# Kernel tuning notes

Measured on AMD Instinct MI355X. Metric: run time of the kernel, lower is better.

## Reference

```python
import jax, jax.numpy as jnp
import numpy as np

REG_TOPK = 4
REG_CHANNELS = 64
ADD_MEAN = True
TOTAL_DIM = REG_TOPK + (1 if ADD_MEAN else 0)  # 5


def setup_inputs() -> dict:
    key = jax.random.key(0)
    k1, k2, k3 = jax.random.split(key, 3)
    N, C, H, W = 32, 32, 160, 160  # C = 4*(reg_max+1), reg_max=7
    x = jax.random.normal(k1, (N, C, H, W), dtype=jnp.float32)
    # 1x1 conv params, init std=0.01, bias 0 (as in torch module)
    w1 = jax.random.normal(k2, (REG_CHANNELS, 4 * TOTAL_DIM), dtype=jnp.float32) * 0.01
    b1 = jnp.zeros((REG_CHANNELS,), dtype=jnp.float32)
    w2 = jax.random.normal(k3, (1, REG_CHANNELS), dtype=jnp.float32) * 0.01
    b2 = jnp.zeros((1,), dtype=jnp.float32)
    return {"x": x, "w1": w1, "b1": b1, "w2": w2, "b2": b2}


def reference(x, w1, b1, w2, b2):
    N, C, H, W = x.shape
    bins = C // 4
    # softmax over distribution bins; move bins to last axis for top_k
    p = jax.nn.softmax(x.reshape(N, 4, bins, H, W), axis=2)  # (N,4,bins,H,W)
    p = jnp.transpose(p, (0, 1, 3, 4, 2))                    # (N,4,H,W,bins)
    topk, _ = jax.lax.top_k(p, REG_TOPK)                     # (N,4,H,W,k)
    if ADD_MEAN:
        stat = jnp.concatenate([topk, topk.mean(axis=-1, keepdims=True)], axis=-1)
    else:
        stat = topk                                          # (N,4,H,W,total_dim)
    # reshape to (N, 4*total_dim, H, W) matching torch layout (4, total_dim contiguous)
    stat = jnp.transpose(stat, (0, 1, 4, 2, 3)).reshape(N, 4 * TOTAL_DIM, H, W)
    y = jax.nn.relu(jnp.einsum('nchw,oc->nohw', stat, w1) + b1[None, :, None, None])
    y = jax.nn.sigmoid(jnp.einsum('nchw,oc->nohw', y, w2) + b2[None, :, None, None])
    return y
```

## Files before the change

kernel.cpp:

```cpp
#include <hip/hip_runtime.h>

#define HW_ 25600
#define CHW_ (32 * 25600)
#define NPIX 819200
#define ROWH 24

typedef _Float16 f16x8 __attribute__((ext_vector_type(8)));
typedef _Float16 h2 __attribute__((ext_vector_type(2)));
typedef float f32x4 __attribute__((ext_vector_type(4)));

__device__ __forceinline__ unsigned short h2us(_Float16 h) {
    return __builtin_bit_cast(unsigned short, h);
}
__device__ __forceinline__ unsigned packlo(h2 a, h2 b) {
    h2 r = {a.x, b.x};
    return __builtin_bit_cast(unsigned, r);
}
__device__ __forceinline__ unsigned packhi(h2 a, h2 b) {
    h2 r = {a.y, b.y};
    return __builtin_bit_cast(unsigned, r);
}
__device__ __forceinline__ h2 pkrtz(float a, float b) {
    return __builtin_bit_cast(h2, __builtin_amdgcn_cvt_pkrtz(a, b));
}

__global__ void dgqp_prep(const float* __restrict__ w1,
                          const float* __restrict__ b1,
                          unsigned short* __restrict__ w1f) {
    int t = threadIdx.x;
    int lane = t & 63;
    int col = ((t >> 6) << 4) | (lane & 15);
    int kg = lane >> 4;
    unsigned int pk[4];
    #pragma unroll
    for (int pr = 0; pr < 4; ++pr) {
        unsigned short hh[2];
        #pragma unroll
        for (int e = 0; e < 2; ++e) {
            int k = kg * 8 + pr * 2 + e;
            float v = 0.f;
            if (k < 16) {
                int g = k >> 2, idx = k & 3;
                v = w1[col * 20 + g * 5 + idx] + 0.25f * w1[col * 20 + g * 5 + 4];
            } else if (k == 16) {
                v = b1[col];
            }
            hh[e] = h2us((_Float16)v);
        }
        pk[pr] = (unsigned int)hh[0] | ((unsigned int)hh[1] << 16);
    }
    *reinterpret_cast<uint4*>(w1f + t * 8) = make_uint4(pk[0], pk[1], pk[2], pk[3]);
}

__global__ __launch_bounds__(256) void dgqp_main(
    const float* __restrict__ x,
    const unsigned short* __restrict__ w1f,
    const float* __restrict__ w2,
    const float* __restrict__ b2,
    float* __restrict__ out)
{
    __shared__ _Float16 lds[512 * ROWH + 8];

    const int tid  = threadIdx.x;
    const int lane = tid & 63;
    const int wpb  = (tid & 192) << 1;
    const int q    = lane & 15;
    const int kg   = lane >> 4;
    const int base = (blockIdx.x * 256 + tid) * 2;
    const unsigned int n = (unsigned int)base / HW_;
    const unsigned int off = (unsigned int)base + n * (unsigned int)(CHW_ - HW_);
    const float* xp = x + off;

    _Float16* row0 = lds + (tid * 2) * ROWH;
    _Float16* row1 = row0 + ROWH;

#define PROC(g, buf) do {                                                    \
        h2 e[8];                                                             \
        _Pragma("unroll")                                                    \
        for (int b = 0; b < 8; ++b)                                          \
            e[b] = pkrtz(__expf(buf[b].x), __expf(buf[b].y));                \
        h2 t0 = (h2)0, t1 = (h2)0, t2 = (h2)0, t3 = (h2)0;                   \
        _Pragma("unroll")                                                    \
        for (int b = 0; b < 8; ++b) {                                        \
            h2 u0 = __builtin_elementwise_min(t0, e[b]);                     \
            t0    = __builtin_elementwise_max(t0, e[b]);                     \
            h2 u1 = __builtin_elementwise_min(t1, u0);                       \
            t1    = __builtin_elementwise_max(t1, u0);                       \
            h2 u2 = __builtin_elementwise_min(t2, u1);                       \
            t2    = __builtin_elementwise_max(t2, u1);                       \
            t3    = __builtin_elementwise_max(t3, u2);                       \
        }                                                                    \
        h2 sum = ((e[0] + e[1]) + (e[2] + e[3])) + ((e[4] + e[5]) + (e[6] + e[7])); \
        float ix = __builtin_amdgcn_rcpf((float)sum.x);                      \
        float iy = __builtin_amdgcn_rcpf((float)sum.y);                      \
        h2 inv = pkrtz(ix, iy);                                              \
        t0 = t0 * inv; t1 = t1 * inv; t2 = t2 * inv; t3 = t3 * inv;          \
        *reinterpret_cast<uint2*>(row0 + (g) * 4) =                          \
            make_uint2(packlo(t0, t1), packlo(t2, t3));                      \
        *reinterpret_cast<uint2*>(row1 + (g) * 4) =                          \
            make_uint2(packhi(t0, t1), packhi(t2, t3));                      \
    } while (0)

    float2 va[8], vb[8];
    #pragma unroll
    for (int b = 0; b < 8; ++b)
        va[b] = *reinterpret_cast<const float2*>(xp + (size_t)b * HW_);
    #pragma unroll
    for (int b = 0; b < 8; ++b)
        vb[b] = *reinterpret_cast<const float2*>(xp + (size_t)(8 + b) * HW_);
    __builtin_amdgcn_sched_barrier(0);
    PROC(0, va);
    #pragma unroll
    for (int b = 0; b < 8; ++b)
        va[b] = *reinterpret_cast<const float2*>(xp + (size_t)(16 + b) * HW_);
    __builtin_amdgcn_sched_barrier(0);
    PROC(1, vb);
    #pragma unroll
    for (int b = 0; b < 8; ++b)
        vb[b] = *reinterpret_cast<const float2*>(xp + (size_t)(24 + b) * HW_);
    __builtin_amdgcn_sched_barrier(0);
    PROC(2, va);
    __builtin_amdgcn_sched_barrier(0);
    PROC(3, vb);
#undef PROC

    const uint4 tail = make_uint4(0x00003C00u, 0u, 0u, 0u);
    *reinterpret_cast<uint4*>(row0 + 16) = tail;
    *reinterpret_cast<uint4*>(row1 + 16) = tail;
    __syncthreads();

    f16x8 bfrag[4];
    #pragma unroll
    for (int nt = 0; nt < 4; ++nt)
        bfrag[nt] = *reinterpret_cast<const f16x8*>(w1f + (nt * 64 + lane) * 8);

    float w2l[4];
    #pragma unroll
    for (int nt = 0; nt < 4; ++nt) w2l[nt] = w2[nt * 16 + q];

    const f32x4 zero4 = {0.f, 0.f, 0.f, 0.f};
    const float bb2 = b2[0];
    const int outbase = blockIdx.x * 512 + wpb;

    #pragma unroll
    for (int m = 0; m < 8; ++m) {
        f16x8 afrag = *reinterpret_cast<const f16x8*>(
            lds + (wpb + m * 16 + q) * ROWH + kg * 8);

        float pm0 = 0.f, pm1 = 0.f, pm2 = 0.f, pm3 = 0.f;
        #pragma unroll
        for (int nt = 0; nt < 4; ++nt) {
            f32x4 d = __builtin_amdgcn_mfma_f32_16x16x32_f16(afrag, bfrag[nt], zero4, 0, 0, 0);
            pm0 = fmaf(w2l[nt], fmaxf(d[0], 0.f), pm0);
            pm1 = fmaf(w2l[nt], fmaxf(d[1], 0.f), pm1);
            pm2 = fmaf(w2l[nt], fmaxf(d[2], 0.f), pm2);
            pm3 = fmaf(w2l[nt], fmaxf(d[3], 0.f), pm3);
        }
        #pragma unroll
        for (int sh = 1; sh < 16; sh <<= 1) {
            pm0 += __shfl_xor(pm0, sh);
            pm1 += __shfl_xor(pm1, sh);
            pm2 += __shfl_xor(pm2, sh);
            pm3 += __shfl_xor(pm3, sh);
        }
        if (q < 4) {
            float r = pm0;
            if (q == 1) r = pm1;
            if (q == 2) r = pm2;
            if (q == 3) r = pm3;
            float y = __builtin_amdgcn_rcpf(1.f + __expf(-(r + bb2)));
            out[outbase + m * 16 + kg * 4 + q] = y;
        }
    }
}

extern "C" void kernel_launch(void* const* d_in, const int* in_sizes, int n_in,
                              void* d_out, int out_size, void* d_ws, size_t ws_size,
                              hipStream_t stream) {
    const float* x  = (const float*)d_in[0];
    const float* w1 = (const float*)d_in[1];
    const float* b1 = (const float*)d_in[2];
    const float* w2 = (const float*)d_in[3];
    const float* b2 = (const float*)d_in[4];
    float* out = (float*)d_out;
    unsigned short* w1f = (unsigned short*)d_ws;

    dgqp_prep<<<1, 256, 0, stream>>>(w1, b1, w1f);
    dgqp_main<<<NPIX / 512, 256, 0, stream>>>(x, w1f, w2, b2, out);
}
```

Baseline: 33.07 us.

## Fuse weight prep into main kernel and transpose MFMA to cut shuffle reduction

Removes the separate single-block weight-preparation launch; each block now builds the fp16 fused w1/b1 fragment itself into shared memory, overlapped after the softmax/top-k phase. The MFMA operands are swapped so output channels lie along rows, letting each lane fold four channels with a vectorised w2 load and needing only two cross-lane shuffles instead of sixteen. The trade-off is redundant per-block weight loads and conversion arithmetic, plus extra LDS use, in exchange for dropping one kernel launch and some reduction work.

After: 28.46 us. 1.16x faster.

```diff
diff --git a/kernel.cpp b/kernel.cpp
--- a/kernel.cpp
+++ b/kernel.cpp
@@ -24,42 +24,16 @@
     return __builtin_bit_cast(h2, __builtin_amdgcn_cvt_pkrtz(a, b));
 }
 
-__global__ void dgqp_prep(const float* __restrict__ w1,
-                          const float* __restrict__ b1,
-                          unsigned short* __restrict__ w1f) {
-    int t = threadIdx.x;
-    int lane = t & 63;
-    int col = ((t >> 6) << 4) | (lane & 15);
-    int kg = lane >> 4;
-    unsigned int pk[4];
-    #pragma unroll
-    for (int pr = 0; pr < 4; ++pr) {
-        unsigned short hh[2];
-        #pragma unroll
-        for (int e = 0; e < 2; ++e) {
-            int k = kg * 8 + pr * 2 + e;
-            float v = 0.f;
-            if (k < 16) {
-                int g = k >> 2, idx = k & 3;
-                v = w1[col * 20 + g * 5 + idx] + 0.25f * w1[col * 20 + g * 5 + 4];
-            } else if (k == 16) {
-                v = b1[col];
-            }
-            hh[e] = h2us((_Float16)v);
-        }
-        pk[pr] = (unsigned int)hh[0] | ((unsigned int)hh[1] << 16);
-    }
-    *reinterpret_cast<uint4*>(w1f + t * 8) = make_uint4(pk[0], pk[1], pk[2], pk[3]);
-}
-
-__global__ __launch_bounds__(256) void dgqp_main(
+__global__ __launch_bounds__(256) void dgqp_fused(
     const float* __restrict__ x,
-    const unsigned short* __restrict__ w1f,
+    const float* __restrict__ w1,
+    const float* __restrict__ b1,
     const float* __restrict__ w2,
     const float* __restrict__ b2,
     float* __restrict__ out)
 {
-    __shared__ _Float16 lds[512 * ROWH + 8];
+    __shared__ _Float16 sstats[512 * ROWH + 8];
+    __shared__ _Float16 swf[2048];
 
     const int tid  = threadIdx.x;
     const int lane = tid & 63;
@@ -71,7 +45,7 @@
     const unsigned int off = (unsigned int)base + n * (unsigned int)(CHW_ - HW_);
     const float* xp = x + off;
 
-    _Float16* row0 = lds + (tid * 2) * ROWH;
+    _Float16* row0 = sstats + (tid * 2) * ROWH;
     _Float16* row1 = row0 + ROWH;
 
 #define PROC(g, buf) do {                                                    \
@@ -124,19 +98,44 @@
     PROC(3, vb);
 #undef PROC
 
+    {
+        const int col = ((tid >> 6) << 4) | (tid & 15);
+        const int kg2 = (tid >> 4) & 3;
+        unsigned int pk[4];
+        #pragma unroll
+        for (int pr = 0; pr < 4; ++pr) {
+            unsigned short hh[2];
+            #pragma unroll
+            for (int e = 0; e < 2; ++e) {
+                int k = kg2 * 8 + pr * 2 + e;
+                float v = 0.f;
+                if (k < 16) {
+                    int g = k >> 2, idx = k & 3;
+                    v = w1[col * 20 + g * 5 + idx] + 0.25f * w1[col * 20 + g * 5 + 4];
+                } else if (k == 16) {
+                    v = b1[col];
+                }
+                hh[e] = h2us((_Float16)v);
+            }
+            pk[pr] = (unsigned int)hh[0] | ((unsigned int)hh[1] << 16);
+        }
+        *reinterpret_cast<uint4*>(swf + tid * 8) = make_uint4(pk[0], pk[1], pk[2], pk[3]);
+    }
+
     const uint4 tail = make_uint4(0x00003C00u, 0u, 0u, 0u);
     *reinterpret_cast<uint4*>(row0 + 16) = tail;
     *reinterpret_cast<uint4*>(row1 + 16) = tail;
     __syncthreads();
 
-    f16x8 bfrag[4];
+    f16x8 wfrag[4];
     #pragma unroll
-    for (int nt = 0; nt < 4; ++nt)
-        bfrag[nt] = *reinterpret_cast<const f16x8*>(w1f + (nt * 64 + lane) * 8);
+    for (int ct = 0; ct < 4; ++ct)
+        wfrag[ct] = *reinterpret_cast<const f16x8*>(swf + (ct * 64 + lane) * 8);
 
-    float w2l[4];
+    f32x4 w2v[4];
     #pragma unroll
-    for (int nt = 0; nt < 4; ++nt) w2l[nt] = w2[nt * 16 + q];
+    for (int ct = 0; ct < 4; ++ct)
+        w2v[ct] = *reinterpret_cast<const f32x4*>(w2 + ct * 16 + kg * 4);
 
     const f32x4 zero4 = {0.f, 0.f, 0.f, 0.f};
     const float bb2 = b2[0];
@@ -144,33 +143,23 @@
 
     #pragma unroll
     for (int m = 0; m < 8; ++m) {
-        f16x8 afrag = *reinterpret_cast<const f16x8*>(
-            lds + (wpb + m * 16 + q) * ROWH + kg * 8);
+        f16x8 sfrag = *reinterpret_cast<const f16x8*>(
+            sstats + (wpb + m * 16 + q) * ROWH + kg * 8);
 
-        float pm0 = 0.f, pm1 = 0.f, pm2 = 0.f, pm3 = 0.f;
+        float pp = 0.f;
         #pragma unroll
-        for (int nt = 0; nt < 4; ++nt) {
-            f32x4 d = __builtin_amdgcn_mfma_f32_16x16x32_f16(afrag, bfrag[nt], zero4, 0, 0, 0);
-            pm0 = fmaf(w2l[nt], fmaxf(d[0], 0.f), pm0);
-            pm1 = fmaf(w2l[nt], fmaxf(d[1], 0.f), pm1);
-            pm2 = fmaf(w2l[nt], fmaxf(d[2], 0.f), pm2);
-            pm3 = fmaf(w2l[nt], fmaxf(d[3], 0.f), pm3);
+        for (int ct = 0; ct < 4; ++ct) {
+            f32x4 d = __builtin_amdgcn_mfma_f32_16x16x32_f16(wfrag[ct], sfrag, zero4, 0, 0, 0);
+            pp = fmaf(w2v[ct][0], fmaxf(d[0], 0.f), pp);
+            pp = fmaf(w2v[ct][1], fmaxf(d[1], 0.f), pp);
+            pp = fmaf(w2v[ct][2], fmaxf(d[2], 0.f), pp);
+            pp = fmaf(w2v[ct][3], fmaxf(d[3], 0.f), pp);
         }
-        #pragma unroll
-        for (int sh = 1; sh < 16; sh <<= 1) {
-            pm0 += __shfl_xor(pm0, sh);
-            pm1 += __shfl_xor(pm1, sh);
-            pm2 += __shfl_xor(pm2, sh);
-            pm3 += __shfl_xor(pm3, sh);
-        }
-        if (q < 4) {
-            float r = pm0;
-            if (q == 1) r = pm1;
-            if (q == 2) r = pm2;
-            if (q == 3) r = pm3;
-            float y = __builtin_amdgcn_rcpf(1.f + __expf(-(r + bb2)));
-            out[outbase + m * 16 + kg * 4 + q] = y;
-        }
+        pp += __shfl_xor(pp, 16);
+        pp += __shfl_xor(pp, 32);
+        float y = __builtin_amdgcn_rcpf(1.f + __expf(-(pp + bb2)));
+        if (lane < 16)
+            out[outbase + m * 16 + q] = y;
     }
 }
 
@@ -183,8 +172,6 @@
     const float* w2 = (const float*)d_in[3];
     const float* b2 = (const float*)d_in[4];
     float* out = (float*)d_out;
-    unsigned short* w1f = (unsigned short*)d_ws;
 
-    dgqp_prep<<<1, 256, 0, stream>>>(w1, b1, w1f);
-    dgqp_main<<<NPIX / 512, 256, 0, stream>>>(x, w1f, w2, b2, out);
+    dgqp_fused<<<NPIX / 512, 256, 0, stream>>>(x, w1, b1, w2, b2, out);
 }
```
